# Performance work log

Hardware: AMD Instinct MI355X
Metric: run time of the kernel (lower is better)

## Reference

```python
import jax, jax.numpy as jnp
import numpy as np


def _lstm_cell(x, h, c, Wih, Whh, b):
    # PyTorch gate order: i, f, g, o
    g = x @ Wih.T + h @ Whh.T + b
    i, f, gg, o = jnp.split(g, 4, axis=-1)
    c2 = jax.nn.sigmoid(f) * c + jax.nn.sigmoid(i) * jnp.tanh(gg)
    h2 = jax.nn.sigmoid(o) * jnp.tanh(c2)
    return h2, c2


def _lstm_seq(x_tbd, h0, c0, Wih, Whh, b):
    # x_tbd: [T, B, D] -> outputs [T, B, H]
    def step(carry, xt):
        h, c = carry
        h2, c2 = _lstm_cell(xt, h, c, Wih, Whh, b)
        return (h2, c2), h2
    _, ys = jax.lax.scan(step, (h0, c0), x_tbd)
    return ys


def setup_inputs() -> dict:
    key = jax.random.key(0)
    ks = jax.random.split(key, 20)
    H, D, A, HOR, NQ = 256, 32, 128, 24, 3
    B, T = 256, 512
    s = 0.1
    inp = {
        'x':      jax.random.normal(ks[0], (B, T, D), jnp.float32),
        'e_Wih0': jax.random.normal(ks[1], (4 * H, D), jnp.float32) * s,
        'e_Whh0': jax.random.normal(ks[2], (4 * H, H), jnp.float32) * s,
        'e_b0':   jax.random.normal(ks[3], (4 * H,), jnp.float32) * s,
        'e_Wih1': jax.random.normal(ks[4], (4 * H, H), jnp.float32) * s,
        'e_Whh1': jax.random.normal(ks[5], (4 * H, H), jnp.float32) * s,
        'e_b1':   jax.random.normal(ks[6], (4 * H,), jnp.float32) * s,
        'd_Wih0': jax.random.normal(ks[7], (4 * H, 1), jnp.float32) * s,
        'd_Whh0': jax.random.normal(ks[8], (4 * H, H), jnp.float32) * s,
        'd_b0':   jax.random.normal(ks[9], (4 * H,), jnp.float32) * s,
        'd_Wih1': jax.random.normal(ks[10], (4 * H, H), jnp.float32) * s,
        'd_Whh1': jax.random.normal(ks[11], (4 * H, H), jnp.float32) * s,
        'd_b1':   jax.random.normal(ks[12], (4 * H,), jnp.float32) * s,
        'aW':     jax.random.normal(ks[13], (H, A), jnp.float32) * s,
        'aV':     jax.random.normal(ks[14], (A,), jnp.float32) * s,
        'qW':     jax.random.normal(ks[15], (NQ, HOR, H), jnp.float32) * s,
        'qb':     jax.random.normal(ks[16], (NQ, HOR), jnp.float32) * s,
    }
    return inp


def reference(x, e_Wih0, e_Whh0, e_b0, e_Wih1, e_Whh1, e_b1,
              d_Wih0, d_Whh0, d_b0, d_Wih1, d_Whh1, d_b1,
              aW, aV, qW, qb):
    B = x.shape[0]
    H = e_Whh0.shape[1]
    horizon = qW.shape[1]

    # ---- encoder: 2-layer LSTM over time ----
    xt = jnp.swapaxes(x, 0, 1)                      # [T, B, D]
    z = jnp.zeros((B, H), x.dtype)
    h1 = _lstm_seq(xt, z, z, e_Wih0, e_Whh0, e_b0)  # [T, B, H]
    h2 = _lstm_seq(h1, z, z, e_Wih1, e_Whh1, e_b1)  # [T, B, H]
    enc = jnp.swapaxes(h2, 0, 1)                    # [B, T, H]

    # ---- attention over encoder outputs ----
    energy = jnp.tanh(enc @ aW) @ aV                # [B, T]
    w = jax.nn.softmax(energy, axis=1)
    context = jnp.einsum('bt,bth->bh', w, enc)      # [B, H]

    inp0 = x[:, -1, -1:]                            # [B, 1]

    def dstep(carry, _):
        h0_, c0_, h1_, c1_, dinp = carry
        h0n, c0n = _lstm_cell(dinp, h0_, c0_, d_Wih0, d_Whh0, d_b0)
        h1n, c1n = _lstm_cell(h0n, h1_, c1_, d_Wih1, d_Whh1, d_b1)
        return (h0n, c0n, h1n, c1n, h1n[:, :1]), h1n

    _, douts = jax.lax.scan(dstep, (context, context, context, context, inp0),
                            None, length=horizon)   # [horizon, B, H]

    # ---- quantile heads on last decoder step ----
    last = douts[-1]                                # [B, H]
    preds = jnp.einsum('bh,qoh->bqo', last, qW) + qb  # [B, n_quantiles, horizon]
    return preds
```

## Files before the change

kernel.cpp:

```cpp
#include <hip/hip_runtime.h>

typedef unsigned short u16;
typedef unsigned int u32;
typedef unsigned long long u64;
typedef short v8s __attribute__((ext_vector_type(8)));
typedef float v4f __attribute__((ext_vector_type(4)));


__device__ __forceinline__ float bf2f(u16 u) { union { u32 u; float f; } c; c.u = ((u32)u) << 16; return c.f; }
__device__ __forceinline__ u16 f2bf(float f) {
  union { float f; u32 u; } c; c.f = f;
  u32 r = c.u + 0x7FFFu + ((c.u >> 16) & 1u);
  return (u16)(r >> 16);
}
__device__ __forceinline__ float sigf(float x) { return 1.f / (1.f + __expf(-x)); }
__device__ __forceinline__ float tanhfast(float x) {
  x = fminf(15.f, fmaxf(-15.f, x));
  float e = __expf(2.f * x);
  return (e - 1.f) / (e + 1.f);
}
__device__ __forceinline__ float ldIn(const void* p, size_t i, int isbf) {
  return isbf ? bf2f(((const u16*)p)[i]) : ((const float*)p)[i];
}
__device__ __forceinline__ v8s ld8hi(const void* p, size_t e, int isbf) {
  if (isbf) return *(const v8s*)((const u16*)p + e);
  const float* f = (const float*)p + e;
  v8s r;
#pragma unroll
  for (int j = 0; j < 8; ++j) r[j] = (short)f2bf(f[j]);
  return r;
}
__device__ __forceinline__ void ld8split(const void* p, size_t e, int isbf, v8s& hi, v8s& lo) {
  if (isbf) {
    hi = *(const v8s*)((const u16*)p + e);
    lo = v8s{0, 0, 0, 0, 0, 0, 0, 0};
  } else {
    const float* f = (const float*)p + e;
#pragma unroll
    for (int j = 0; j < 8; ++j) {
      u16 h = f2bf(f[j]);
      hi[j] = (short)h;
      lo[j] = (short)f2bf(f[j] - bf2f(h));
    }
  }
}
#define MFMA(a, b, c) __builtin_amdgcn_mfma_f32_16x16x32_bf16(a, b, c, 0, 0, 0)

__device__ __forceinline__ u64 aload64(const u64* p) {
  return __hip_atomic_load(p, __ATOMIC_RELAXED, __HIP_MEMORY_SCOPE_AGENT);
}
__device__ __forceinline__ void astore64(u64* p, u64 v) {
  __hip_atomic_store(p, v, __ATOMIC_RELAXED, __HIP_MEMORY_SCOPE_AGENT);
}

__device__ __forceinline__ void stage_dec(u16* dhi, u16* dlo, const u64* src,
                                          int tid, u32 tag) {
  u64 v[16];
#pragma unroll
  for (int i = 0; i < 16; ++i) v[i] = aload64(src + i * 256 + tid);
  bool all;
  do {
    all = true;
#pragma unroll
    for (int i = 0; i < 16; ++i) {
      if ((u32)(v[i] >> 32) != tag) { all = false; v[i] = aload64(src + i * 256 + tid); }
    }
  } while (!all);
#pragma unroll
  for (int i = 0; i < 16; ++i) {
    int idx = i * 256 + tid;
    int row = idx >> 8, col = idx & 255;
    dhi[row * 264 + col] = (u16)v[i];
    dlo[row * 264 + col] = (u16)(v[i] >> 16);
  }
}
__device__ __forceinline__ void stage_f32(u16* dhi, u16* dlo, const float* src, int tid) {
#pragma unroll
  for (int i = 0; i < 8; ++i) {
    int e = i * 512 + tid * 2;
    int row = e >> 8, jc = e & 255;
    float f0 = src[row * 256 + jc], f1 = src[row * 256 + jc + 1];
    u16 h0 = f2bf(f0), h1 = f2bf(f1);
    u16 l0 = f2bf(f0 - bf2f(h0)), l1 = f2bf(f1 - bf2f(h1));
    ((u32*)(dhi + row * 264))[jc >> 1] = (u32)h0 | ((u32)h1 << 16);
    ((u32*)(dlo + row * 264))[jc >> 1] = (u32)l0 | ((u32)l1 << 16);
  }
}

__global__ void sniff_kernel(const u16* __restrict__ w, int* __restrict__ flag) {
  __shared__ int cnt;
  if (threadIdx.x == 0) cnt = 0;
  __syncthreads();
  int ok = 0;
  for (int i = threadIdx.x; i < 1024; i += 256) {
    u16 u = w[2 * i];
    int e = (u >> 7) & 0xFF;
    ok += (u == 0 || (e >= 97 && e <= 140)) ? 1 : 0;
  }
  atomicAdd(&cnt, ok);
  __syncthreads();
  if (threadIdx.x == 0) *flag = (cnt >= 768) ? 1 : 0;
}

__global__ __launch_bounds__(256, 1) void enc_kernel(
    const void* __restrict__ x,
    const void* __restrict__ eWih0, const void* __restrict__ eWhh0, const void* __restrict__ eb0,
    const void* __restrict__ eWih1, const void* __restrict__ eWhh1, const void* __restrict__ eb1,
    const void* __restrict__ aW, const void* __restrict__ aV,
    u64* __restrict__ C,
    float* __restrict__ ctx, const int* __restrict__ flagp) {
  __shared__ __align__(16) u16 h0s[16 * 264], h1s[16 * 264];
  __shared__ float gb0[16 * 64], gb1[16 * 64];
  __shared__ float eP[2][16 * 132];

  const int isbf = *flagp;
  const int tid = threadIdx.x, blk = blockIdx.x;
  const int grp = blk & 15, gs = blk >> 4;
  const int lane = tid & 63, wv = tid >> 6;
  const int ln = lane & 15, lq = lane >> 4;

  v8s W0F[9], W1F[16], AWF[16];
  {
    const int gw = wv * 256 + gs * 16 + ln;
    const int kq = lq * 8;
    W0F[0] = ld8hi(eWih0, (size_t)gw * 32 + kq, isbf);
#pragma unroll
    for (int kt = 0; kt < 8; ++kt) {
      W0F[kt + 1] = ld8hi(eWhh0, (size_t)gw * 256 + kt * 32 + kq, isbf);
      W1F[kt]     = ld8hi(eWhh1, (size_t)gw * 256 + kt * 32 + kq, isbf);
      W1F[kt + 8] = ld8hi(eWih1, (size_t)gw * 256 + kt * 32 + kq, isbf);
    }
#pragma unroll
    for (int kt = 0; kt < 8; ++kt)
#pragma unroll
      for (int j2 = 0; j2 < 2; ++j2) {
        v8s f;
        int ac = (2 * wv + j2) * 16 + ln;
#pragma unroll
        for (int j = 0; j < 8; ++j)
          f[j] = (short)f2bf(ldIn(aW, (size_t)(kt * 32 + kq + j) * 128 + ac, isbf));
        AWF[kt * 2 + j2] = f;
      }
  }

  const int urow = tid >> 4, uu = tid & 15;
  float bg0[4], bg1[4], aVr[8];
#pragma unroll
  for (int g = 0; g < 4; ++g) {
    bg0[g] = ldIn(eb0, g * 256 + gs * 16 + uu, isbf);
    bg1[g] = ldIn(eb1, g * 256 + gs * 16 + uu, isbf);
  }
#pragma unroll
  for (int j = 0; j < 8; ++j) aVr[j] = ldIn(aV, (size_t)(uu + 16 * j), isbf);

  const int gRowU = grp * 16 + urow;
  const int gUnit = gs * 16 + uu;
  const int aRow = grp * 16 + ln;
  const u32 stOff = (u32)(grp * 4096 + gs * 256 + urow * 16 + uu);

  float c0 = 0.f, c1 = 0.f;
  float mS = -3e38f, lS = 0.f, ctxA = 0.f;
  float h1v = 0.f;

  v8s xh_c, xl_c;
  ld8split(x, ((size_t)aRow * 512) * 32 + lq * 8, isbf, xh_c, xl_c);
  v8s a0r[8], a1r[8];

#pragma unroll 1
  for (int t = 0; t < 514; ++t) {
    const int rPar = (t + 1) & 1, wPar = t & 1;
    const u32 tag = (u32)(u16)t;
    {
      const u64* src = C + (size_t)rPar * 65536 + grp * 4096;
      u64 v[16];
#pragma unroll
      for (int i = 0; i < 16; ++i) v[i] = aload64(src + i * 256 + tid);
      bool all;
      do {
        all = true;
#pragma unroll
        for (int i = 0; i < 16; ++i) {
          u64 w = v[i];
          if (!((((w >> 16) & 0xFFFFull) == tag) && ((w >> 48) == tag))) {
            all = false;
            v[i] = aload64(src + i * 256 + tid);
          }
        }
      } while (!all);
#pragma unroll
      for (int i = 0; i < 16; ++i) {
        u64 w = v[i];
        h0s[urow * 264 + i * 16 + uu] = (u16)w;
        h1s[urow * 264 + i * 16 + uu] = (u16)(w >> 32);
      }
    }
    __syncthreads();

#pragma unroll
    for (int kt = 0; kt < 8; ++kt) {
      const int off = ln * 264 + kt * 32 + lq * 8;
      a0r[kt] = *(const v8s*)(h0s + off);
      a1r[kt] = *(const v8s*)(h1s + off);
    }
    if (t < 512) {
      v4f A = {0, 0, 0, 0}, B = {0, 0, 0, 0};
      A = MFMA(xh_c, W0F[0], A);
      if (!isbf) A = MFMA(xl_c, W0F[0], A);
#pragma unroll
      for (int kt = 0; kt < 4; ++kt) A = MFMA(a0r[kt], W0F[kt + 1], A);
#pragma unroll
      for (int kt = 4; kt < 8; ++kt) B = MFMA(a0r[kt], W0F[kt + 1], B);
#pragma unroll
      for (int r = 0; r < 4; ++r) gb0[(lq * 4 + r) * 64 + ln * 4 + wv] = A[r] + B[r];
    }
    {
      v4f A = {0, 0, 0, 0}, B = {0, 0, 0, 0};
#pragma unroll
      for (int kt = 0; kt < 8; ++kt) {
        A = MFMA(a0r[kt], W1F[kt + 8], A);
        B = MFMA(a1r[kt], W1F[kt], B);
      }
#pragma unroll
      for (int r = 0; r < 4; ++r) gb1[(lq * 4 + r) * 64 + ln * 4 + wv] = A[r] + B[r];
    }
    __syncthreads();

    const u32 tagS = (u32)(u16)(t + 1) << 16;
    if (t <= 512) {
      u32 w0 = tagS, w1 = tagS;
      if (t < 512) {
        const float* g0 = gb0 + (urow * 16 + uu) * 4;
        float gi = g0[0] + bg0[0], gf = g0[1] + bg0[1], gg = g0[2] + bg0[2], go = g0[3] + bg0[3];
        c0 = sigf(gf) * c0 + sigf(gi) * tanhfast(gg);
        float h = sigf(go) * tanhfast(c0);
        w0 |= (u32)f2bf(h);
      }
      if (t >= 1) {
        const float* g1 = gb1 + (urow * 16 + uu) * 4;
        float gi = g1[0] + bg1[0], gf = g1[1] + bg1[1], gg = g1[2] + bg1[2], go = g1[3] + bg1[3];
        c1 = sigf(gf) * c1 + sigf(gi) * tanhfast(gg);
        float h = sigf(go) * tanhfast(c1);
        w1 |= (u32)f2bf(h);
      }
      astore64(C + (size_t)wPar * 65536 + stOff, (u64)w0 | ((u64)w1 << 32));
    }

    if (t >= 3) {
      const float* ep = eP[(t + 1) & 1];
      float e = 0.f;
#pragma unroll
      for (int j = 0; j < 8; ++j)
        e += tanhfast(ep[urow * 132 + uu + 16 * j]) * aVr[j];
      e += __shfl_xor(e, 1);
      e += __shfl_xor(e, 2);
      e += __shfl_xor(e, 4);
      e += __shfl_xor(e, 8);
      float nm = fmaxf(mS, e);
      float al = __expf(mS - nm), p = __expf(e - nm);
      lS = lS * al + p;
      ctxA = ctxA * al + p * h1v;
      mS = nm;
    }
    if (t >= 2) {
      v4f A = {0, 0, 0, 0}, B = {0, 0, 0, 0};
#pragma unroll
      for (int kt = 0; kt < 8; ++kt) {
        A = MFMA(a1r[kt], AWF[kt * 2], A);
        B = MFMA(a1r[kt], AWF[kt * 2 + 1], B);
      }
      float* ep = eP[t & 1];
#pragma unroll
      for (int r = 0; r < 4; ++r) {
        ep[(lq * 4 + r) * 132 + (2 * wv) * 16 + ln] = A[r];
        ep[(lq * 4 + r) * 132 + (2 * wv + 1) * 16 + ln] = B[r];
      }
      h1v = bf2f(h1s[urow * 264 + gUnit]);
    }
    {
      int tn = (t + 1 < 512) ? t + 1 : 511;
      ld8split(x, ((size_t)aRow * 512 + tn) * 32 + lq * 8, isbf, xh_c, xl_c);
    }
  }
  __syncthreads();
  {
    const float* ep = eP[1];
    float e = 0.f;
#pragma unroll
    for (int j = 0; j < 8; ++j)
      e += tanhfast(ep[urow * 132 + uu + 16 * j]) * aVr[j];
    e += __shfl_xor(e, 1);
    e += __shfl_xor(e, 2);
    e += __shfl_xor(e, 4);
    e += __shfl_xor(e, 8);
    float nm = fmaxf(mS, e);
    float al = __expf(mS - nm), p = __expf(e - nm);
    lS = lS * al + p;
    ctxA = ctxA * al + p * h1v;
    mS = nm;
  }
  ctx[(size_t)gRowU * 256 + gUnit] = ctxA / lS;
}

__global__ __launch_bounds__(256, 1) void dec_kernel(
    const void* __restrict__ x,
    const void* __restrict__ dWih0, const void* __restrict__ dWhh0, const void* __restrict__ db0,
    const void* __restrict__ dWih1, const void* __restrict__ dWhh1, const void* __restrict__ db1,
    const void* __restrict__ qW, const void* __restrict__ qb,
    const float* __restrict__ ctx,
    u64* __restrict__ H0d, u64* __restrict__ H1d, u64* __restrict__ dinpG,
    void* __restrict__ out, const int* __restrict__ flagp) {
  __shared__ u16 sAhi[16 * 264], sAlo[16 * 264], sBhi[16 * 264], sBlo[16 * 264];
  __shared__ float gb[16 * 64];
  __shared__ float dinpS[16];

  const int isbf = *flagp;
  const int tid = threadIdx.x, blk = blockIdx.x;
  const int grp = blk & 15, gs = blk >> 4;
  const int lane = tid & 63, wv = tid >> 6;
  const int ln = lane & 15, lq = lane >> 4;

  v8s W0F[8], W1F[16];
  {
    const int gw = wv * 256 + gs * 16 + ln;
    const int kq = lq * 8;
#pragma unroll
    for (int kt = 0; kt < 8; ++kt) {
      W0F[kt]     = ld8hi(dWhh0, (size_t)gw * 256 + kt * 32 + kq, isbf);
      W1F[kt]     = ld8hi(dWhh1, (size_t)gw * 256 + kt * 32 + kq, isbf);
      W1F[kt + 8] = ld8hi(dWih1, (size_t)gw * 256 + kt * 32 + kq, isbf);
    }
  }
  const int urow = tid >> 4, uu = tid & 15;
  float bg0[4], bg1[4], w0v[4];
#pragma unroll
  for (int g = 0; g < 4; ++g) {
    bg0[g] = ldIn(db0, g * 256 + gs * 16 + uu, isbf);
    bg1[g] = ldIn(db1, g * 256 + gs * 16 + uu, isbf);
    w0v[g] = ldIn(dWih0, g * 256 + gs * 16 + uu, isbf);
  }
  const int gRowU = grp * 16 + urow;
  const int gUnit = gs * 16 + uu;

  float c0 = ctx[(size_t)gRowU * 256 + gUnit];
  float c1 = c0;

#pragma unroll 1
  for (int t = 0; t < 24; ++t) {
    const int pPrev = (t + 1) & 1, pCur = t & 1;
    if (t == 0) {
      stage_f32(sAhi, sAlo, ctx + (size_t)grp * 16 * 256, tid);
      if (tid < 16)
        dinpS[tid] = ldIn(x, ((size_t)(grp * 16 + tid) * 512 + 511) * 32 + 31, isbf);
    } else {
      stage_dec(sAhi, sAlo, H0d + (size_t)pPrev * 65536 + grp * 4096, tid, (u32)(2 * t - 1));
      if (tid < 16) {
        u64 w;
        do { w = aload64(dinpG + pPrev * 256 + grp * 16 + tid); } while ((u32)(w >> 32) != (u32)(2 * t));
        dinpS[tid] = __uint_as_float((u32)w);
      }
    }
    __syncthreads();
    v4f acc = {0, 0, 0, 0};
#pragma unroll
    for (int kt = 0; kt < 8; ++kt) {
      const int off = ln * 264 + kt * 32 + lq * 8;
      acc = MFMA(*(const v8s*)(sAhi + off), W0F[kt], acc);
      acc = MFMA(*(const v8s*)(sAlo + off), W0F[kt], acc);
    }
    {
      const int bR = lq * 4;
#pragma unroll
      for (int r = 0; r < 4; ++r) gb[(bR + r) * 64 + ln * 4 + wv] = acc[r];
    }
    float di = dinpS[urow];
    __syncthreads();
    {
      const float* g0 = gb + (urow * 16 + uu) * 4;
      float gi = g0[0] + bg0[0] + di * w0v[0];
      float gf = g0[1] + bg0[1] + di * w0v[1];
      float gg = g0[2] + bg0[2] + di * w0v[2];
      float go = g0[3] + bg0[3] + di * w0v[3];
      c0 = sigf(gf) * c0 + sigf(gi) * tanhfast(gg);
      float h = sigf(go) * tanhfast(c0);
      u16 hh = f2bf(h); u16 hl = f2bf(h - bf2f(hh));
      astore64(H0d + (size_t)pCur * 65536 + gRowU * 256 + gUnit,
               (u64)hh | ((u64)hl << 16) | ((u64)(u32)(2 * t + 1) << 32));
    }
    if (t == 0) stage_f32(sBhi, sBlo, ctx + (size_t)grp * 16 * 256, tid);
    else stage_dec(sBhi, sBlo, H1d + (size_t)pPrev * 65536 + grp * 4096, tid, (u32)(2 * t));
    stage_dec(sAhi, sAlo, H0d + (size_t)pCur * 65536 + grp * 4096, tid, (u32)(2 * t + 1));
    __syncthreads();
    v4f a1 = {0, 0, 0, 0};
#pragma unroll
    for (int kt = 0; kt < 8; ++kt) {
      const int off = ln * 264 + kt * 32 + lq * 8;
      a1 = MFMA(*(const v8s*)(sBhi + off), W1F[kt], a1);
      a1 = MFMA(*(const v8s*)(sBlo + off), W1F[kt], a1);
      a1 = MFMA(*(const v8s*)(sAhi + off), W1F[kt + 8], a1);
      a1 = MFMA(*(const v8s*)(sAlo + off), W1F[kt + 8], a1);
    }
    {
      const int bR = lq * 4;
#pragma unroll
      for (int r = 0; r < 4; ++r) gb[(bR + r) * 64 + ln * 4 + wv] = a1[r];
    }
    __syncthreads();
    {
      const float* g1 = gb + (urow * 16 + uu) * 4;
      float gi = g1[0] + bg1[0], gf = g1[1] + bg1[1], gg = g1[2] + bg1[2], go = g1[3] + bg1[3];
      c1 = sigf(gf) * c1 + sigf(gi) * tanhfast(gg);
      float h = sigf(go) * tanhfast(c1);
      u16 hh = f2bf(h); u16 hl = f2bf(h - bf2f(hh));
      astore64(H1d + (size_t)pCur * 65536 + gRowU * 256 + gUnit,
               (u64)hh | ((u64)hl << 16) | ((u64)(u32)(2 * t + 2) << 32));
      if (gUnit == 0)
        astore64(dinpG + pCur * 256 + gRowU,
                 (u64)__float_as_uint(h) | ((u64)(u32)(2 * t + 2) << 32));
    }
  }
  stage_dec(sAhi, sAlo, H1d + (size_t)65536 + grp * 4096, tid, 48u);
  __syncthreads();
  if (gs < 12 && tid < 96) {
    int r = tid / 6, p = tid % 6;
    int qo = gs * 6 + p, row = grp * 16 + r;
    float s = ldIn(qb, qo, isbf);
    for (int h = 0; h < 256; ++h)
      s += (bf2f(sAhi[r * 264 + h]) + bf2f(sAlo[r * 264 + h])) * ldIn(qW, (size_t)qo * 256 + h, isbf);
    if (isbf) ((u16*)out)[row * 72 + qo] = f2bf(s);
    else      ((float*)out)[row * 72 + qo] = s;
  }
}

extern "C" void kernel_launch(void* const* d_in, const int* in_sizes, int n_in,
                              void* d_out, int out_size, void* d_ws, size_t ws_size,
                              hipStream_t stream) {
  const void* x     = d_in[0];
  const void* eWih0 = d_in[1];
  const void* eWhh0 = d_in[2];
  const void* eb0   = d_in[3];
  const void* eWih1 = d_in[4];
  const void* eWhh1 = d_in[5];
  const void* eb1   = d_in[6];
  const void* dWih0 = d_in[7];
  const void* dWhh0 = d_in[8];
  const void* db0   = d_in[9];
  const void* dWih1 = d_in[10];
  const void* dWhh1 = d_in[11];
  const void* db1   = d_in[12];
  const void* aW    = d_in[13];
  const void* aV    = d_in[14];
  const void* qW    = d_in[15];
  const void* qb    = d_in[16];

  char* wsb = (char*)d_ws;
  u64*   C     = (u64*)(wsb + 0);
  u64*   H0d   = (u64*)(wsb + 1048576);
  u64*   H1d   = (u64*)(wsb + 2097152);
  u64*   dinpG = (u64*)(wsb + 3145728);
  int*   flag  = (int*)(wsb + 3149824);
  float* ctx   = (float*)(wsb + 3150080);

  hipMemsetAsync(wsb, 0, 3149824, stream);

  sniff_kernel<<<1, 256, 0, stream>>>((const u16*)eWhh0, flag);
  enc_kernel<<<256, 256, 0, stream>>>(x, eWih0, eWhh0, eb0, eWih1, eWhh1, eb1,
                                      aW, aV, C, ctx, flag);
  dec_kernel<<<256, 256, 0, stream>>>(x, dWih0, dWhh0, db0, dWih1, dWhh1, db1,
                                      qW, qb, ctx, H0d, H1d, dinpG,
                                      d_out, flag);
}
```

Measured before the change: 2.053 ms.

## Prefetch next-step exchange buffer and ping-pong two in-flight poll loads

Issues the poll loads for the next timestep's cross-block exchange buffer early, right after this step's store, so they are in flight during the attention work. The spin-wait now alternates between two in-flight load sets, so polling latency overlaps instead of serialising reload-then-check. The intent is to cut cross-block synchronisation latency on the recurrent critical path. In exchange it uses more registers for the extra 16 u64 values, and the early loads often return stale tags that must be reloaded.

```diff
diff --git a/kernel.cpp b/kernel.cpp
--- a/kernel.cpp
+++ b/kernel.cpp
@@ -166,30 +166,43 @@
   ld8split(x, ((size_t)aRow * 512) * 32 + lq * 8, isbf, xh_c, xl_c);
   v8s a0r[8], a1r[8];
 
+  u64 vA[16];
+  {
+    const u64* src0 = C + (size_t)1 * 65536 + grp * 4096;
+#pragma unroll
+    for (int i = 0; i < 16; ++i) vA[i] = aload64(src0 + i * 256 + tid);
+  }
+
 #pragma unroll 1
   for (int t = 0; t < 514; ++t) {
     const int rPar = (t + 1) & 1, wPar = t & 1;
     const u32 tag = (u32)(u16)t;
+    const u64 exp64 = ((u64)tag << 16) | ((u64)tag << 48);
     {
       const u64* src = C + (size_t)rPar * 65536 + grp * 4096;
-      u64 v[16];
-#pragma unroll
-      for (int i = 0; i < 16; ++i) v[i] = aload64(src + i * 256 + tid);
-      bool all;
-      do {
-        all = true;
-#pragma unroll
-        for (int i = 0; i < 16; ++i) {
-          u64 w = v[i];
-          if (!((((w >> 16) & 0xFFFFull) == tag) && ((w >> 48) == tag))) {
-            all = false;
-            v[i] = aload64(src + i * 256 + tid);
-          }
-        }
-      } while (!all);
+      u64 vB[16];
+#pragma unroll
+      for (int i = 0; i < 16; ++i) vB[i] = aload64(src + i * 256 + tid);
+      bool gotB = false;
+      while (true) {
+        bool ok = true;
+#pragma unroll
+        for (int i = 0; i < 16; ++i)
+          ok &= (((vA[i] ^ exp64) & 0xFFFF0000FFFF0000ull) == 0);
+        if (ok) break;
+#pragma unroll
+        for (int i = 0; i < 16; ++i) vA[i] = aload64(src + i * 256 + tid);
+        ok = true;
+#pragma unroll
+        for (int i = 0; i < 16; ++i)
+          ok &= (((vB[i] ^ exp64) & 0xFFFF0000FFFF0000ull) == 0);
+        if (ok) { gotB = true; break; }
+#pragma unroll
+        for (int i = 0; i < 16; ++i) vB[i] = aload64(src + i * 256 + tid);
+      }
 #pragma unroll
       for (int i = 0; i < 16; ++i) {
-        u64 w = v[i];
+        u64 w = gotB ? vB[i] : vA[i];
         h0s[urow * 264 + i * 16 + uu] = (u16)w;
         h1s[urow * 264 + i * 16 + uu] = (u16)(w >> 32);
       }
@@ -243,6 +256,12 @@
         w1 |= (u32)f2bf(h);
       }
       astore64(C + (size_t)wPar * 65536 + stOff, (u64)w0 | ((u64)w1 << 32));
+    }
+
+    if (t < 513) {
+      const u64* nsrc = C + (size_t)(t & 1) * 65536 + grp * 4096;
+#pragma unroll
+      for (int i = 0; i < 16; ++i) vA[i] = aload64(nsrc + i * 256 + tid);
     }
 
     if (t >= 3) {
```

Result: slower. 2.397 ms (+16.8%).

## Split encoder block into recurrence waves and attention/x-prefetch waves

Applied to the files above, without the earlier changes.

The encoder block grows from 256 to 512 threads and is warp-specialized. Waves 0-3 run only the two-layer LSTM recurrence and the cross-block hidden-state exchange. Waves 4-7 run the attention energy MFMAs and the online softmax context, and stage the next timestep's x into double-buffered shared memory. This takes the attention work and the per-step global x loads off the latency-bound recurrent critical path. In exchange, every block-wide barrier now spans eight waves, and the two branches must issue exactly the same number of barriers to stay correct.

```diff
diff --git a/kernel.cpp b/kernel.cpp
--- a/kernel.cpp
+++ b/kernel.cpp
@@ -29,20 +29,6 @@
 #pragma unroll
   for (int j = 0; j < 8; ++j) r[j] = (short)f2bf(f[j]);
   return r;
-}
-__device__ __forceinline__ void ld8split(const void* p, size_t e, int isbf, v8s& hi, v8s& lo) {
-  if (isbf) {
-    hi = *(const v8s*)((const u16*)p + e);
-    lo = v8s{0, 0, 0, 0, 0, 0, 0, 0};
-  } else {
-    const float* f = (const float*)p + e;
-#pragma unroll
-    for (int j = 0; j < 8; ++j) {
-      u16 h = f2bf(f[j]);
-      hi[j] = (short)h;
-      lo[j] = (short)f2bf(f[j] - bf2f(h));
-    }
-  }
 }
 #define MFMA(a, b, c) __builtin_amdgcn_mfma_f32_16x16x32_bf16(a, b, c, 0, 0, 0)
 
@@ -102,7 +88,7 @@
   if (threadIdx.x == 0) *flag = (cnt >= 768) ? 1 : 0;
 }
 
-__global__ __launch_bounds__(256, 1) void enc_kernel(
+__global__ __launch_bounds__(512, 1) void enc_kernel(
     const void* __restrict__ x,
     const void* __restrict__ eWih0, const void* __restrict__ eWhh0, const void* __restrict__ eb0,
     const void* __restrict__ eWih1, const void* __restrict__ eWhh1, const void* __restrict__ eb1,
@@ -111,194 +97,226 @@
     float* __restrict__ ctx, const int* __restrict__ flagp) {
   __shared__ __align__(16) u16 h0s[16 * 264], h1s[16 * 264];
   __shared__ float gb0[16 * 64], gb1[16 * 64];
-  __shared__ float eP[2][16 * 132];
+  __shared__ float eP[16 * 132];
+  __shared__ __align__(16) u16 xsh[2][16 * 40], xsl[2][16 * 40];
 
   const int isbf = *flagp;
   const int tid = threadIdx.x, blk = blockIdx.x;
   const int grp = blk & 15, gs = blk >> 4;
-  const int lane = tid & 63, wv = tid >> 6;
+  const int wv8 = tid >> 6;
+  const int lane = tid & 63;
   const int ln = lane & 15, lq = lane >> 4;
 
-  v8s W0F[9], W1F[16], AWF[16];
-  {
-    const int gw = wv * 256 + gs * 16 + ln;
-    const int kq = lq * 8;
-    W0F[0] = ld8hi(eWih0, (size_t)gw * 32 + kq, isbf);
-#pragma unroll
-    for (int kt = 0; kt < 8; ++kt) {
-      W0F[kt + 1] = ld8hi(eWhh0, (size_t)gw * 256 + kt * 32 + kq, isbf);
-      W1F[kt]     = ld8hi(eWhh1, (size_t)gw * 256 + kt * 32 + kq, isbf);
-      W1F[kt + 8] = ld8hi(eWih1, (size_t)gw * 256 + kt * 32 + kq, isbf);
-    }
-#pragma unroll
-    for (int kt = 0; kt < 8; ++kt)
-#pragma unroll
-      for (int j2 = 0; j2 < 2; ++j2) {
-        v8s f;
-        int ac = (2 * wv + j2) * 16 + ln;
-#pragma unroll
-        for (int j = 0; j < 8; ++j)
-          f[j] = (short)f2bf(ldIn(aW, (size_t)(kt * 32 + kq + j) * 128 + ac, isbf));
-        AWF[kt * 2 + j2] = f;
-      }
-  }
-
-  const int urow = tid >> 4, uu = tid & 15;
-  float bg0[4], bg1[4], aVr[8];
-#pragma unroll
-  for (int g = 0; g < 4; ++g) {
-    bg0[g] = ldIn(eb0, g * 256 + gs * 16 + uu, isbf);
-    bg1[g] = ldIn(eb1, g * 256 + gs * 16 + uu, isbf);
-  }
-#pragma unroll
-  for (int j = 0; j < 8; ++j) aVr[j] = ldIn(aV, (size_t)(uu + 16 * j), isbf);
-
-  const int gRowU = grp * 16 + urow;
-  const int gUnit = gs * 16 + uu;
-  const int aRow = grp * 16 + ln;
-  const u32 stOff = (u32)(grp * 4096 + gs * 256 + urow * 16 + uu);
-
-  float c0 = 0.f, c1 = 0.f;
-  float mS = -3e38f, lS = 0.f, ctxA = 0.f;
-  float h1v = 0.f;
-
-  v8s xh_c, xl_c;
-  ld8split(x, ((size_t)aRow * 512) * 32 + lq * 8, isbf, xh_c, xl_c);
-  v8s a0r[8], a1r[8];
+  if (wv8 < 4) {
+    const int wv = wv8;
+    v8s W0F[9], W1F[16];
+    {
+      const int gw = wv * 256 + gs * 16 + ln;
+      const int kq = lq * 8;
+      W0F[0] = ld8hi(eWih0, (size_t)gw * 32 + kq, isbf);
+#pragma unroll
+      for (int kt = 0; kt < 8; ++kt) {
+        W0F[kt + 1] = ld8hi(eWhh0, (size_t)gw * 256 + kt * 32 + kq, isbf);
+        W1F[kt]     = ld8hi(eWhh1, (size_t)gw * 256 + kt * 32 + kq, isbf);
+        W1F[kt + 8] = ld8hi(eWih1, (size_t)gw * 256 + kt * 32 + kq, isbf);
+      }
+    }
+    const int urow = tid >> 4, uu = tid & 15;
+    float bg0[4], bg1[4];
+#pragma unroll
+    for (int g = 0; g < 4; ++g) {
+      bg0[g] = ldIn(eb0, g * 256 + gs * 16 + uu, isbf);
+      bg1[g] = ldIn(eb1, g * 256 + gs * 16 + uu, isbf);
+    }
+    const u32 stOff = (u32)(grp * 4096 + gs * 256 + urow * 16 + uu);
+    float c0 = 0.f, c1 = 0.f;
+    v8s a0r[8], a1r[8];
+
+    __syncthreads();
 
 #pragma unroll 1
-  for (int t = 0; t < 514; ++t) {
-    const int rPar = (t + 1) & 1, wPar = t & 1;
-    const u32 tag = (u32)(u16)t;
-    {
-      const u64* src = C + (size_t)rPar * 65536 + grp * 4096;
-      u64 v[16];
-#pragma unroll
-      for (int i = 0; i < 16; ++i) v[i] = aload64(src + i * 256 + tid);
-      bool all;
-      do {
-        all = true;
+    for (int t = 0; t < 514; ++t) {
+      const int rPar = (t + 1) & 1, wPar = t & 1;
+      const u32 tag = (u32)(u16)t;
+      {
+        const u64* src = C + (size_t)rPar * 65536 + grp * 4096;
+        u64 v[16];
+#pragma unroll
+        for (int i = 0; i < 16; ++i) v[i] = aload64(src + i * 256 + tid);
+        bool all;
+        do {
+          all = true;
+#pragma unroll
+          for (int i = 0; i < 16; ++i) {
+            u64 w = v[i];
+            if (!((((w >> 16) & 0xFFFFull) == tag) && ((w >> 48) == tag))) {
+              all = false;
+              v[i] = aload64(src + i * 256 + tid);
+            }
+          }
+        } while (!all);
 #pragma unroll
         for (int i = 0; i < 16; ++i) {
           u64 w = v[i];
-          if (!((((w >> 16) & 0xFFFFull) == tag) && ((w >> 48) == tag))) {
-            all = false;
-            v[i] = aload64(src + i * 256 + tid);
-          }
-        }
-      } while (!all);
-#pragma unroll
-      for (int i = 0; i < 16; ++i) {
-        u64 w = v[i];
-        h0s[urow * 264 + i * 16 + uu] = (u16)w;
-        h1s[urow * 264 + i * 16 + uu] = (u16)(w >> 32);
-      }
-    }
-    __syncthreads();
-
-#pragma unroll
-    for (int kt = 0; kt < 8; ++kt) {
-      const int off = ln * 264 + kt * 32 + lq * 8;
-      a0r[kt] = *(const v8s*)(h0s + off);
-      a1r[kt] = *(const v8s*)(h1s + off);
-    }
-    if (t < 512) {
-      v4f A = {0, 0, 0, 0}, B = {0, 0, 0, 0};
-      A = MFMA(xh_c, W0F[0], A);
-      if (!isbf) A = MFMA(xl_c, W0F[0], A);
-#pragma unroll
-      for (int kt = 0; kt < 4; ++kt) A = MFMA(a0r[kt], W0F[kt + 1], A);
-#pragma unroll
-      for (int kt = 4; kt < 8; ++kt) B = MFMA(a0r[kt], W0F[kt + 1], B);
-#pragma unroll
-      for (int r = 0; r < 4; ++r) gb0[(lq * 4 + r) * 64 + ln * 4 + wv] = A[r] + B[r];
-    }
-    {
-      v4f A = {0, 0, 0, 0}, B = {0, 0, 0, 0};
+          h0s[urow * 264 + i * 16 + uu] = (u16)w;
+          h1s[urow * 264 + i * 16 + uu] = (u16)(w >> 32);
+        }
+      }
+      __syncthreads();
+
 #pragma unroll
       for (int kt = 0; kt < 8; ++kt) {
-        A = MFMA(a0r[kt], W1F[kt + 8], A);
-        B = MFMA(a1r[kt], W1F[kt], B);
-      }
-#pragma unroll
-      for (int r = 0; r < 4; ++r) gb1[(lq * 4 + r) * 64 + ln * 4 + wv] = A[r] + B[r];
-    }
-    __syncthreads();
-
-    const u32 tagS = (u32)(u16)(t + 1) << 16;
-    if (t <= 512) {
-      u32 w0 = tagS, w1 = tagS;
+        const int off = ln * 264 + kt * 32 + lq * 8;
+        a0r[kt] = *(const v8s*)(h0s + off);
+        a1r[kt] = *(const v8s*)(h1s + off);
+      }
       if (t < 512) {
-        const float* g0 = gb0 + (urow * 16 + uu) * 4;
-        float gi = g0[0] + bg0[0], gf = g0[1] + bg0[1], gg = g0[2] + bg0[2], go = g0[3] + bg0[3];
-        c0 = sigf(gf) * c0 + sigf(gi) * tanhfast(gg);
-        float h = sigf(go) * tanhfast(c0);
-        w0 |= (u32)f2bf(h);
-      }
-      if (t >= 1) {
-        const float* g1 = gb1 + (urow * 16 + uu) * 4;
-        float gi = g1[0] + bg1[0], gf = g1[1] + bg1[1], gg = g1[2] + bg1[2], go = g1[3] + bg1[3];
-        c1 = sigf(gf) * c1 + sigf(gi) * tanhfast(gg);
-        float h = sigf(go) * tanhfast(c1);
-        w1 |= (u32)f2bf(h);
-      }
-      astore64(C + (size_t)wPar * 65536 + stOff, (u64)w0 | ((u64)w1 << 32));
-    }
-
-    if (t >= 3) {
-      const float* ep = eP[(t + 1) & 1];
-      float e = 0.f;
-#pragma unroll
-      for (int j = 0; j < 8; ++j)
-        e += tanhfast(ep[urow * 132 + uu + 16 * j]) * aVr[j];
-      e += __shfl_xor(e, 1);
-      e += __shfl_xor(e, 2);
-      e += __shfl_xor(e, 4);
-      e += __shfl_xor(e, 8);
-      float nm = fmaxf(mS, e);
-      float al = __expf(mS - nm), p = __expf(e - nm);
-      lS = lS * al + p;
-      ctxA = ctxA * al + p * h1v;
-      mS = nm;
-    }
-    if (t >= 2) {
-      v4f A = {0, 0, 0, 0}, B = {0, 0, 0, 0};
-#pragma unroll
-      for (int kt = 0; kt < 8; ++kt) {
-        A = MFMA(a1r[kt], AWF[kt * 2], A);
-        B = MFMA(a1r[kt], AWF[kt * 2 + 1], B);
-      }
-      float* ep = eP[t & 1];
-#pragma unroll
-      for (int r = 0; r < 4; ++r) {
-        ep[(lq * 4 + r) * 132 + (2 * wv) * 16 + ln] = A[r];
-        ep[(lq * 4 + r) * 132 + (2 * wv + 1) * 16 + ln] = B[r];
-      }
-      h1v = bf2f(h1s[urow * 264 + gUnit]);
-    }
-    {
-      int tn = (t + 1 < 512) ? t + 1 : 511;
-      ld8split(x, ((size_t)aRow * 512 + tn) * 32 + lq * 8, isbf, xh_c, xl_c);
-    }
-  }
-  __syncthreads();
-  {
-    const float* ep = eP[1];
-    float e = 0.f;
-#pragma unroll
-    for (int j = 0; j < 8; ++j)
-      e += tanhfast(ep[urow * 132 + uu + 16 * j]) * aVr[j];
-    e += __shfl_xor(e, 1);
-    e += __shfl_xor(e, 2);
-    e += __shfl_xor(e, 4);
-    e += __shfl_xor(e, 8);
-    float nm = fmaxf(mS, e);
-    float al = __expf(mS - nm), p = __expf(e - nm);
-    lS = lS * al + p;
-    ctxA = ctxA * al + p * h1v;
-    mS = nm;
-  }
-  ctx[(size_t)gRowU * 256 + gUnit] = ctxA / lS;
+        v8s xh = *(const v8s*)(xsh[t & 1] + ln * 40 + lq * 8);
+        v4f A = {0, 0, 0, 0}, B = {0, 0, 0, 0};
+        A = MFMA(xh, W0F[0], A);
+        if (!isbf) {
+          v8s xl = *(const v8s*)(xsl[t & 1] + ln * 40 + lq * 8);
+          A = MFMA(xl, W0F[0], A);
+        }
+#pragma unroll
+        for (int kt = 0; kt < 4; ++kt) A = MFMA(a0r[kt], W0F[kt + 1], A);
+#pragma unroll
+        for (int kt = 4; kt < 8; ++kt) B = MFMA(a0r[kt], W0F[kt + 1], B);
+#pragma unroll
+        for (int r = 0; r < 4; ++r) gb0[(lq * 4 + r) * 64 + ln * 4 + wv] = A[r] + B[r];
+      }
+      {
+        v4f A = {0, 0, 0, 0}, B = {0, 0, 0, 0};
+#pragma unroll
+        for (int kt = 0; kt < 8; ++kt) {
+          A = MFMA(a0r[kt], W1F[kt + 8], A);
+          B = MFMA(a1r[kt], W1F[kt], B);
+        }
+#pragma unroll
+        for (int r = 0; r < 4; ++r) gb1[(lq * 4 + r) * 64 + ln * 4 + wv] = A[r] + B[r];
+      }
+      __syncthreads();
+
+      const u32 tagS = (u32)(u16)(t + 1) << 16;
+      if (t <= 512) {
+        u32 w0 = tagS, w1 = tagS;
+        if (t < 512) {
+          const float* g0 = gb0 + (urow * 16 + uu) * 4;
+          float gi = g0[0] + bg0[0], gf = g0[1] + bg0[1], gg = g0[2] + bg0[2], go = g0[3] + bg0[3];
+          c0 = sigf(gf) * c0 + sigf(gi) * tanhfast(gg);
+          float h = sigf(go) * tanhfast(c0);
+          w0 |= (u32)f2bf(h);
+        }
+        if (t >= 1) {
+          const float* g1 = gb1 + (urow * 16 + uu) * 4;
+          float gi = g1[0] + bg1[0], gf = g1[1] + bg1[1], gg = g1[2] + bg1[2], go = g1[3] + bg1[3];
+          c1 = sigf(gf) * c1 + sigf(gi) * tanhfast(gg);
+          float h = sigf(go) * tanhfast(c1);
+          w1 |= (u32)f2bf(h);
+        }
+        astore64(C + (size_t)wPar * 65536 + stOff, (u64)w0 | ((u64)w1 << 32));
+      }
+    }
+  } else {
+    const int aw = wv8 - 4;
+    v8s AWF[16];
+    {
+      const int kq = lq * 8;
+#pragma unroll
+      for (int kt = 0; kt < 8; ++kt)
+#pragma unroll
+        for (int j2 = 0; j2 < 2; ++j2) {
+          v8s f;
+          int ac = (2 * aw + j2) * 16 + ln;
+#pragma unroll
+          for (int j = 0; j < 8; ++j)
+            f[j] = (short)f2bf(ldIn(aW, (size_t)(kt * 32 + kq + j) * 128 + ac, isbf));
+          AWF[kt * 2 + j2] = f;
+        }
+    }
+    const int tid2 = tid - 256;
+    const int urow2 = tid2 >> 4, uu2 = tid2 & 15;
+    const int gUnit2 = gs * 16 + uu2;
+    float aVr[8];
+#pragma unroll
+    for (int j = 0; j < 8; ++j) aVr[j] = ldIn(aV, (size_t)(uu2 + 16 * j), isbf);
+
+    float mS = -3e38f, lS = 0.f, ctxA = 0.f;
+
+    const int xe = tid2 * 2, xrow = xe >> 5, xcol = xe & 31;
+    const size_t xbase = ((size_t)(grp * 16 + xrow) * 512) * 32 + xcol;
+
+    {
+      if (isbf) {
+        u32 v = *(const u32*)((const u16*)x + xbase);
+        *(u32*)(xsh[0] + xrow * 40 + xcol) = v;
+        *(u32*)(xsl[0] + xrow * 40 + xcol) = 0;
+      } else {
+        const float* f = (const float*)x + xbase;
+        float f0 = f[0], f1 = f[1];
+        u16 h0 = f2bf(f0), h1 = f2bf(f1);
+        u16 l0 = f2bf(f0 - bf2f(h0)), l1 = f2bf(f1 - bf2f(h1));
+        *(u32*)(xsh[0] + xrow * 40 + xcol) = (u32)h0 | ((u32)h1 << 16);
+        *(u32*)(xsl[0] + xrow * 40 + xcol) = (u32)l0 | ((u32)l1 << 16);
+      }
+    }
+    __syncthreads();
+
+#pragma unroll 1
+    for (int t = 0; t < 514; ++t) {
+      if (t < 511) {
+        const int par = (t + 1) & 1;
+        const size_t off = xbase + (size_t)(t + 1) * 32;
+        if (isbf) {
+          u32 v = *(const u32*)((const u16*)x + off);
+          *(u32*)(xsh[par] + xrow * 40 + xcol) = v;
+        } else {
+          const float* f = (const float*)x + off;
+          float f0 = f[0], f1 = f[1];
+          u16 h0 = f2bf(f0), h1 = f2bf(f1);
+          u16 l0 = f2bf(f0 - bf2f(h0)), l1 = f2bf(f1 - bf2f(h1));
+          *(u32*)(xsh[par] + xrow * 40 + xcol) = (u32)h0 | ((u32)h1 << 16);
+          *(u32*)(xsl[par] + xrow * 40 + xcol) = (u32)l0 | ((u32)l1 << 16);
+        }
+      }
+      __syncthreads();
+
+      float h1v = 0.f;
+      if (t >= 2) {
+        v4f A = {0, 0, 0, 0}, B = {0, 0, 0, 0};
+#pragma unroll
+        for (int kt = 0; kt < 8; ++kt) {
+          v8s a1 = *(const v8s*)(h1s + ln * 264 + kt * 32 + lq * 8);
+          A = MFMA(a1, AWF[kt * 2], A);
+          B = MFMA(a1, AWF[kt * 2 + 1], B);
+        }
+#pragma unroll
+        for (int r = 0; r < 4; ++r) {
+          eP[(lq * 4 + r) * 132 + (2 * aw) * 16 + ln] = A[r];
+          eP[(lq * 4 + r) * 132 + (2 * aw + 1) * 16 + ln] = B[r];
+        }
+        h1v = bf2f(h1s[urow2 * 264 + gUnit2]);
+      }
+      __syncthreads();
+
+      if (t >= 2) {
+        float e = 0.f;
+#pragma unroll
+        for (int j = 0; j < 8; ++j)
+          e += tanhfast(eP[urow2 * 132 + uu2 + 16 * j]) * aVr[j];
+        e += __shfl_xor(e, 1);
+        e += __shfl_xor(e, 2);
+        e += __shfl_xor(e, 4);
+        e += __shfl_xor(e, 8);
+        float nm = fmaxf(mS, e);
+        float al = __expf(mS - nm), p = __expf(e - nm);
+        lS = lS * al + p;
+        ctxA = ctxA * al + p * h1v;
+        mS = nm;
+      }
+    }
+    ctx[(size_t)(grp * 16 + urow2) * 256 + gUnit2] = ctxA / lS;
+  }
 }
 
 __global__ __launch_bounds__(256, 1) void dec_kernel(
@@ -463,7 +481,7 @@
   hipMemsetAsync(wsb, 0, 3149824, stream);
 
   sniff_kernel<<<1, 256, 0, stream>>>((const u16*)eWhh0, flag);
-  enc_kernel<<<256, 256, 0, stream>>>(x, eWih0, eWhh0, eb0, eWih1, eWhh1, eb1,
+  enc_kernel<<<256, 512, 0, stream>>>(x, eWih0, eWhh0, eb0, eWih1, eWhh1, eb1,
                                       aW, aV, C, ctx, flag);
   dec_kernel<<<256, 256, 0, stream>>>(x, dWih0, dWhh0, db0, dWih1, dWhh1, db1,
                                       qW, qb, ctx, H0d, H1d, dinpG,
```

Result: no change. 2.088 ms (+1.7%).
